# Kernel optimization log

Measured on AMD Instinct MI355X. Metric: run time of the kernel, lower is better.

Reference implementation:

```python
import jax, jax.numpy as jnp
import numpy as np

B, P, M, N, H = 2, 2048, 1024, 16, 64
NEG = 1e10


def setup_inputs() -> dict:
    key = jax.random.key(0)
    ks = jax.random.split(key, 8)
    std = 0.02
    return {
        "x": jax.random.normal(ks[0], (B, P, M), jnp.float32),
        "kernel_query": std * jax.random.normal(ks[1], (N, M, H), jnp.float32),
        "bias_query": jnp.zeros((N, H), jnp.float32),
        "kernel_key": std * jax.random.normal(ks[2], (N, M, H), jnp.float32),
        "bias_key": jnp.zeros((N, H), jnp.float32),
        "kernel_value": std * jax.random.normal(ks[3], (N, M, H), jnp.float32),
        "bias_value": jnp.zeros((N, H), jnp.float32),
        "kernel_out": std * jax.random.normal(ks[4], (N, H, M), jnp.float32),
        "bias_out": jnp.zeros((M,), jnp.float32),
    }


def reference(x, kernel_query, bias_query, kernel_key, bias_key,
              kernel_value, bias_value, kernel_out, bias_out):
    # per-head projections: [b,p,m] x [n,m,h] -> [b,p,n,h]
    q = jnp.einsum('bpm,nmh->bpnh', x, kernel_query) + bias_query
    k = jnp.einsum('bpm,nmh->bpnh', x, kernel_key) + bias_key
    v = jnp.einsum('bpm,nmh->bpnh', x, kernel_value) + bias_value

    # explicit score matrix [b,n,pq,pk]
    scores = jnp.einsum('bqnh,bknh->bnqk', q, k) / jnp.sqrt(jnp.float32(H))
    # faithful reproduction of original (inverted) mask: keep strictly-upper
    # triangle, subtract 1e10 elsewhere
    p = scores.shape[-1]
    mask = jnp.triu(jnp.ones((p, p), scores.dtype), k=1)  # [pq,pk]
    masked = scores * mask - NEG * (1.0 - mask)
    attn = jax.nn.softmax(masked, axis=-1)

    z = jnp.einsum('bknh,bnqk->bqnh', v, attn)
    return jnp.einsum('bqnh,nhm->bqm', z, kernel_out) + bias_out
```

## Files before the change

### kernel.cpp

```cpp
#include <hip/hip_runtime.h>

typedef __attribute__((ext_vector_type(8))) __bf16 bf16x8;
typedef __attribute__((ext_vector_type(4))) float  f32x4;
typedef unsigned short u16;
typedef unsigned int   u32;

__device__ __forceinline__ u16 f2b(float f) {
  u32 u = __builtin_bit_cast(u32, f);
  u32 r = (u + 0x7FFFu + ((u >> 16) & 1u)) >> 16;
  return (u16)r;
}

typedef __attribute__((address_space(3))) void lds_void;
typedef const __attribute__((address_space(1))) void gbl_void;

__device__ __forceinline__ void gload_lds16(const u16* g, u16* l) {
  __builtin_amdgcn_global_load_lds((gbl_void*)g, (lds_void*)l, 16, 0, 0);
}

#define QSCALE 0.18033688011112042f
#define MFIX   4.328085122666891f

__global__ __launch_bounds__(256) void prep_x(const float* __restrict__ x,
                                              u16* __restrict__ xb) {
  int i = blockIdx.x * 256 + threadIdx.x;
  float4 v = ((const float4*)x)[i];
  ushort4 o;
  o.x = f2b(v.x); o.y = f2b(v.y); o.z = f2b(v.z); o.w = f2b(v.w);
  ((ushort4*)xb)[i] = o;
}

__global__ __launch_bounds__(256) void tcast(const float* __restrict__ src,
                                             u16* __restrict__ dst,
                                             int R, int C, int sstride, int dstride,
                                             int smat, int dmat) {
  __shared__ float t[64][65];
  src += (size_t)blockIdx.y * smat;
  dst += (size_t)blockIdx.y * dmat;
  int ntr = R >> 6;
  int rt = blockIdx.x % ntr, ct = blockIdx.x / ntr;
  int r0 = rt * 64, c0 = ct * 64;
  int tid = threadIdx.x;
  int rr = tid >> 2, q = tid & 3;
#pragma unroll
  for (int i = 0; i < 4; ++i) {
    float4 v = *(const float4*)&src[(size_t)(r0 + rr) * sstride + c0 + q * 16 + i * 4];
    t[rr][q * 16 + i * 4 + 0] = v.x;
    t[rr][q * 16 + i * 4 + 1] = v.y;
    t[rr][q * 16 + i * 4 + 2] = v.z;
    t[rr][q * 16 + i * 4 + 3] = v.w;
  }
  __syncthreads();
  int cc = rr;
#pragma unroll
  for (int i = 0; i < 4; ++i) {
    ushort4 o;
    o.x = f2b(t[q * 16 + i * 4 + 0][cc]);
    o.y = f2b(t[q * 16 + i * 4 + 1][cc]);
    o.z = f2b(t[q * 16 + i * 4 + 2][cc]);
    o.w = f2b(t[q * 16 + i * 4 + 3][cc]);
    *(ushort4*)&dst[(size_t)(c0 + cc) * dstride + r0 + q * 16 + i * 4] = o;
  }
}

template <int KDIM>
__device__ __forceinline__ void gemm_main(const u16* __restrict__ A,
                                          const u16* __restrict__ Bm,
                                          int R0, int C0,
                                          u16* As, u16* Bs, f32x4 (&acc)[4][4]) {
  int tid = threadIdx.x;
  int w = tid >> 6, l = tid & 63;
  int lr = l & 15, lg = l >> 4;
  int wr = w >> 1, wc = w & 1;
  for (int k0 = 0; k0 < KDIM; k0 += 32) {
#pragma unroll
    for (int i = 0; i < 2; ++i) {
      int t = w * 2 + i;
      gload_lds16(A  + (size_t)(R0 + t * 16 + (l >> 2)) * KDIM + k0 + (l & 3) * 8, &As[t * 512]);
      gload_lds16(Bm + (size_t)(C0 + t * 16 + (l >> 2)) * KDIM + k0 + (l & 3) * 8, &Bs[t * 512]);
    }
    __syncthreads();
    bf16x8 af[4], bfr[4];
#pragma unroll
    for (int mi = 0; mi < 4; ++mi)
      af[mi] = *(const bf16x8*)&As[(wr * 64 + mi * 16 + lr) * 32 + lg * 8];
#pragma unroll
    for (int ni = 0; ni < 4; ++ni)
      bfr[ni] = *(const bf16x8*)&Bs[(wc * 64 + ni * 16 + lr) * 32 + lg * 8];
#pragma unroll
    for (int mi = 0; mi < 4; ++mi)
#pragma unroll
      for (int ni = 0; ni < 4; ++ni)
        acc[mi][ni] = __builtin_amdgcn_mfma_f32_16x16x32_bf16(af[mi], bfr[ni], acc[mi][ni], 0, 0, 0);
    __syncthreads();
  }
}

__global__ __launch_bounds__(256) void gemm_qkv(const u16* __restrict__ xb,
                                                const u16* __restrict__ wbt,
                                                const float* __restrict__ bq,
                                                const float* __restrict__ bk,
                                                const float* __restrict__ bv,
                                                u16* __restrict__ qb,
                                                u16* __restrict__ kbf,
                                                u16* __restrict__ vtb) {
  __shared__ __align__(16) u16 As[128 * 32];
  __shared__ __align__(16) u16 Bs[128 * 32];
  f32x4 acc[4][4];
#pragma unroll
  for (int mi = 0; mi < 4; ++mi)
#pragma unroll
    for (int ni = 0; ni < 4; ++ni) acc[mi][ni] = (f32x4){0.f, 0.f, 0.f, 0.f};

  int bid = blockIdx.x;
  int rt = bid & 31, ct = bid >> 5;
  int R0 = rt * 128, C0 = ct * 128;
  gemm_main<1024>(xb, wbt, R0, C0, As, Bs, acc);

  int tid = threadIdx.x;
  int w = tid >> 6, l = tid & 63;
  int lr = l & 15, lg = l >> 4;
  int wr = w >> 1, wc = w & 1;
#pragma unroll
  for (int ni = 0; ni < 4; ++ni) {
    int col = C0 + wc * 64 + ni * 16 + lr;
    int proj = col >> 10;
    int within = col & 1023;
    int n = within >> 6, h = within & 63;
    const float* bias = (proj == 0) ? bq : (proj == 1 ? bk : bv);
    float badd = bias[within];
    float scl = (proj == 0) ? QSCALE : 1.0f;
#pragma unroll
    for (int mi = 0; mi < 4; ++mi) {
#pragma unroll
      for (int r = 0; r < 4; ++r) {
        int row = R0 + wr * 64 + mi * 16 + lg * 4 + r;
        int b = row >> 11, p = row & 2047;
        int bn = b * 16 + n;
        u16 u = f2b((acc[mi][ni][r] + badd) * scl);
        if (proj == 0)      qb [((size_t)bn * 2048 + p) * 64 + h] = u;
        else if (proj == 1) kbf[((size_t)bn * 2048 + p) * 64 + h] = u;
        else                vtb[(((size_t)bn * 32 + (p >> 6)) * 64 + h) * 64 + (p & 63)] = u;
      }
    }
  }
}

__global__ __launch_bounds__(256) void mean_v(const u16* __restrict__ vtb,
                                              u16* __restrict__ zb) {
  __shared__ float red[4][64];
  int bn = blockIdx.x;
  int w = threadIdx.x >> 6, h = threadIdx.x & 63;
  const u16* base = vtb + (size_t)bn * 131072 + (size_t)h * 64;
  float acc = 0.f;
  for (int pb = w; pb < 32; pb += 4) {
    const u16* r = base + (size_t)pb * 4096;
#pragma unroll
    for (int c = 0; c < 8; ++c) {
      bf16x8 v = *(const bf16x8*)(r + c * 8);
#pragma unroll
      for (int j = 0; j < 8; ++j) acc += (float)v[j];
    }
  }
  red[w][h] = acc;
  __syncthreads();
  if (w == 0) {
    float s = (red[0][h] + red[1][h] + red[2][h] + red[3][h]) * (1.0f / 2048.0f);
    int b = bn >> 4, n = bn & 15;
    zb[((size_t)(b * 2048 + 2047) * 16 + n) * 64 + h] = f2b(s);
  }
}

#define ATTN_STEP(BUFC, VM, DO_STAGE)                                          \
  {                                                                            \
    asm volatile("s_waitcnt vmcnt(" #VM ")" ::: "memory");                     \
    __builtin_amdgcn_s_barrier();                                              \
    asm volatile("" ::: "memory");                                             \
    f32x4 sacc[4];                                                             \
    __builtin_amdgcn_s_setprio(1);                                             \
    _Pragma("unroll") for (int nb = 0; nb < 4; ++nb) {                         \
      int row = nb * 16 + lr, sw = row & 7;                                    \
      bf16x8 kf0 = *(const bf16x8*)&Ks[BUFC][row * 64 + ((lg ^ sw) << 3)];     \
      bf16x8 kf1 = *(const bf16x8*)&Ks[BUFC][row * 64 + (((lg + 4) ^ sw) << 3)]; \
      f32x4 s = (f32x4){0.f, 0.f, 0.f, 0.f};                                   \
      s = __builtin_amdgcn_mfma_f32_16x16x32_bf16(qf0, kf0, s, 0, 0, 0);       \
      s = __builtin_amdgcn_mfma_f32_16x16x32_bf16(qf1, kf1, s, 0, 0, 0);       \
      sacc[nb] = s;                                                            \
    }                                                                          \
    __builtin_amdgcn_s_setprio(0);                                             \
    u16 pbv[4][4];                                                             \
    if (kb < q0w + 16) {                                                       \
      _Pragma("unroll") for (int nb = 0; nb < 4; ++nb) {                       \
        int key = kb + nb * 16 + lr;                                           \
        _Pragma("unroll") for (int r = 0; r < 4; ++r) {                        \
          int qrow = q0w + lg * 4 + r;                                         \
          float xv = (key > qrow) ? sacc[nb][r] : -1.0e10f;                    \
          float pe = __builtin_amdgcn_exp2f(xv - MFIX);                        \
          rsum[r] += pe;                                                       \
          pbv[nb][r] = __builtin_bit_cast(u16, (__bf16)pe);                    \
        }                                                                      \
      }                                                                        \
    } else {                                                                   \
      _Pragma("unroll") for (int nb = 0; nb < 4; ++nb)                         \
        _Pragma("unroll") for (int r = 0; r < 4; ++r) {                        \
          float pe = __builtin_amdgcn_exp2f(sacc[nb][r] - MFIX);               \
          rsum[r] += pe;                                                       \
          pbv[nb][r] = __builtin_bit_cast(u16, (__bf16)pe);                    \
        }                                                                      \
    }                                                                          \
    _Pragma("unroll") for (int nb = 0; nb < 4; ++nb)                           \
      _Pragma("unroll") for (int r = 0; r < 4; ++r)                            \
        Plds[w][lg * 4 + r][nb * 16 + lr] = pbv[nb][r];                        \
    asm volatile("s_waitcnt lgkmcnt(0)" ::: "memory");                         \
    __builtin_amdgcn_sched_barrier(0);                                         \
    bf16x8 pf0 = *(const bf16x8*)&Plds[w][lr][lg * 8];                         \
    bf16x8 pf1 = *(const bf16x8*)&Plds[w][lr][32 + lg * 8];                    \
    __builtin_amdgcn_s_setprio(1);                                             \
    _Pragma("unroll") for (int hb = 0; hb < 4; ++hb) {                         \
      int row = hb * 16 + lr, sw = row & 7;                                    \
      bf16x8 vf0 = *(const bf16x8*)&Vs[BUFC][row * 64 + ((lg ^ sw) << 3)];     \
      bf16x8 vf1 = *(const bf16x8*)&Vs[BUFC][row * 64 + (((lg + 4) ^ sw) << 3)]; \
      oacc[hb] = __builtin_amdgcn_mfma_f32_16x16x32_bf16(pf0, vf0, oacc[hb], 0, 0, 0); \
      oacc[hb] = __builtin_amdgcn_mfma_f32_16x16x32_bf16(pf1, vf1, oacc[hb], 0, 0, 0); \
    }                                                                          \
    __builtin_amdgcn_s_setprio(0);                                             \
    if (t == tA - 1) {                                                         \
      finalize(q0w);                                                           \
      q0w = cB * 64 + w * 16;                                                  \
      qf0 = *(const bf16x8*)&Q[(size_t)(q0w + lr) * 64 + lg * 8];              \
      qf1 = *(const bf16x8*)&Q[(size_t)(q0w + lr) * 64 + 32 + lg * 8];         \
      _Pragma("unroll") for (int r = 0; r < 4; ++r) rsum[r] = 0.0f;            \
      _Pragma("unroll") for (int hb = 0; hb < 4; ++hb)                         \
        oacc[hb] = (f32x4){0.f, 0.f, 0.f, 0.f};                                \
      kb = cB * 64 - 64;                                                       \
    }                                                                          \
    asm volatile("" ::: "memory");                                             \
    __builtin_amdgcn_s_barrier();                                              \
    if (DO_STAGE) {                                                            \
      if (t + 3 == tA) {                                                       \
        sk = Kp + (size_t)cB * 4096 + soff;                                    \
        sv = Vt + (size_t)cB * 4096 + soff;                                    \
      }                                                                        \
      gload_lds16(sk,       &Ks[BUFC][w * 1024]);                              \
      gload_lds16(sk + 512, &Ks[BUFC][w * 1024 + 512]);                        \
      gload_lds16(sv,       &Vs[BUFC][w * 1024]);                              \
      gload_lds16(sv + 512, &Vs[BUFC][w * 1024 + 512]);                        \
      sk += 4096; sv += 4096;                                                  \
    }                                                                          \
    kb += 64; ++t;                                                             \
  }

__global__ __launch_bounds__(256) void attn_kern(const u16* __restrict__ qb,
                                                 const u16* __restrict__ kbf,
                                                 const u16* __restrict__ vtb,
                                                 u16* __restrict__ zb) {
  __shared__ __align__(16) u16 Ks[3][4096];
  __shared__ __align__(16) u16 Vs[3][4096];
  __shared__ __align__(16) u16 Plds[4][16][72];

  int bid = blockIdx.x;
  int bn = bid & 31, p = bid >> 5;
  int tid = threadIdx.x;
  int w = tid >> 6, l = tid & 63;
  int lr = l & 15, lg = l >> 4;

  int cA = p, cB = 31 - p;
  int tA = 32 - p;

  const u16* Q  = qb  + (size_t)bn * 131072;
  const u16* Kp = kbf + (size_t)bn * 131072;
  const u16* Vt = vtb + (size_t)bn * 131072;

  int row0 = w * 16 + (l >> 3), col8 = l & 7;
  int soff = row0 * 64 + ((col8 ^ (row0 & 7)) << 3);

  int q0w = cA * 64 + w * 16;
  bf16x8 qf0 = *(const bf16x8*)&Q[(size_t)(q0w + lr) * 64 + lg * 8];
  bf16x8 qf1 = *(const bf16x8*)&Q[(size_t)(q0w + lr) * 64 + 32 + lg * 8];

  float rsum[4];
  f32x4 oacc[4];
#pragma unroll
  for (int r = 0; r < 4; ++r) rsum[r] = 0.0f;
#pragma unroll
  for (int hb = 0; hb < 4; ++hb) oacc[hb] = (f32x4){0.f, 0.f, 0.f, 0.f};

  auto finalize = [&](int q0) {
#pragma unroll
    for (int r = 0; r < 4; ++r) {
      float v = rsum[r];
      v += __shfl_xor(v, 1);
      v += __shfl_xor(v, 2);
      v += __shfl_xor(v, 4);
      v += __shfl_xor(v, 8);
      rsum[r] = 1.0f / v;
    }
    int b = bn >> 4, n = bn & 15;
#pragma unroll
    for (int hb = 0; hb < 4; ++hb) {
      int h = hb * 16 + lr;
#pragma unroll
      for (int r = 0; r < 4; ++r) {
        int qrow = q0 + lg * 4 + r;
        zb[((size_t)(b * 2048 + qrow) * 16 + n) * 64 + h] = f2b(oacc[hb][r] * rsum[r]);
      }
    }
  };

  const u16* sk = Kp + (size_t)cA * 4096 + soff;
  const u16* sv = Vt + (size_t)cA * 4096 + soff;
#pragma unroll
  for (int i = 0; i < 3; ++i) {
    gload_lds16(sk,       &Ks[i][w * 1024]);
    gload_lds16(sk + 512, &Ks[i][w * 1024 + 512]);
    gload_lds16(sv,       &Vs[i][w * 1024]);
    gload_lds16(sv + 512, &Vs[i][w * 1024 + 512]);
    sk += 4096; sv += 4096;
  }

  int t = 0;
  int kb = cA * 64;
  for (int it = 0; it < 10; ++it) {
    ATTN_STEP(0, 8, true)
    ATTN_STEP(1, 8, true)
    ATTN_STEP(2, 8, true)
  }
  ATTN_STEP(0, 8, false)
  ATTN_STEP(1, 4, false)
  ATTN_STEP(2, 0, false)
  finalize(q0w);
}

__global__ __launch_bounds__(256) void gemm_out(const u16* __restrict__ zb,
                                                const u16* __restrict__ wot,
                                                const float* __restrict__ bo,
                                                float* __restrict__ out) {
  __shared__ __align__(16) u16 As[128 * 32];
  __shared__ __align__(16) u16 Bs[128 * 32];
  f32x4 acc[4][4];
#pragma unroll
  for (int mi = 0; mi < 4; ++mi)
#pragma unroll
    for (int ni = 0; ni < 4; ++ni) acc[mi][ni] = (f32x4){0.f, 0.f, 0.f, 0.f};

  int bid = blockIdx.x;
  int rt = bid & 31, ct = bid >> 5;
  int R0 = rt * 128, C0 = ct * 128;
  gemm_main<1024>(zb, wot, R0, C0, As, Bs, acc);

  int tid = threadIdx.x;
  int w = tid >> 6, l = tid & 63;
  int lr = l & 15, lg = l >> 4;
  int wr = w >> 1, wc = w & 1;
#pragma unroll
  for (int ni = 0; ni < 4; ++ni) {
    int col = C0 + wc * 64 + ni * 16 + lr;
    float badd = bo[col];
#pragma unroll
    for (int mi = 0; mi < 4; ++mi) {
#pragma unroll
      for (int r = 0; r < 4; ++r) {
        int row = R0 + wr * 64 + mi * 16 + lg * 4 + r;
        out[(size_t)row * 1024 + col] = acc[mi][ni][r] + badd;
      }
    }
  }
}

extern "C" void kernel_launch(void* const* d_in, const int* in_sizes, int n_in,
                              void* d_out, int out_size, void* d_ws, size_t ws_size,
                              hipStream_t stream) {
  const float* x  = (const float*)d_in[0];
  const float* wq = (const float*)d_in[1];
  const float* bq = (const float*)d_in[2];
  const float* wk = (const float*)d_in[3];
  const float* bk = (const float*)d_in[4];
  const float* wv = (const float*)d_in[5];
  const float* bv = (const float*)d_in[6];
  const float* wo = (const float*)d_in[7];
  const float* bo = (const float*)d_in[8];
  float* out = (float*)d_out;

  char* ws = (char*)d_ws;
  u16* xb  = (u16*)(ws + ((size_t)0 << 20));
  u16* wbt = (u16*)(ws + ((size_t)8 << 20));
  u16* wot = (u16*)(ws + ((size_t)14 << 20));
  u16* qb  = (u16*)(ws + ((size_t)16 << 20));
  u16* kbf = (u16*)(ws + ((size_t)24 << 20));
  u16* vtb = (u16*)(ws + ((size_t)32 << 20));
  u16* zb  = (u16*)(ws + ((size_t)40 << 20));

  prep_x<<<dim3(4096), dim3(256), 0, stream>>>(x, xb);
  tcast<<<dim3(16, 16), dim3(256), 0, stream>>>(wq, wbt + (0u << 20), 1024, 64, 64, 1024, 65536, 65536);
  tcast<<<dim3(16, 16), dim3(256), 0, stream>>>(wk, wbt + (1u << 20), 1024, 64, 64, 1024, 65536, 65536);
  tcast<<<dim3(16, 16), dim3(256), 0, stream>>>(wv, wbt + (2u << 20), 1024, 64, 64, 1024, 65536, 65536);
  tcast<<<dim3(256, 1), dim3(256), 0, stream>>>(wo, wot, 1024, 1024, 1024, 1024, 0, 0);

  gemm_qkv<<<dim3(32 * 24), dim3(256), 0, stream>>>(xb, wbt, bq, bk, bv, qb, kbf, vtb);
  attn_kern<<<dim3(512), dim3(256), 0, stream>>>(qb, kbf, vtb, zb);
  mean_v<<<dim3(32), dim3(256), 0, stream>>>(vtb, zb);
  gemm_out<<<dim3(32 * 8), dim3(256), 0, stream>>>(zb, wot, bo, out);
}
```

Baseline: 131.4 us.

## Split paired-chunk attention blocks into one block per query chunk with double buffering

```diff
diff --git a/kernel.cpp b/kernel.cpp
--- a/kernel.cpp
+++ b/kernel.cpp
@@ -171,9 +171,18 @@
   }
 }
 
-#define ATTN_STEP(BUFC, VM, DO_STAGE)                                          \
+#define ATTN_STEP(BUFC, MASKED)                                                \
   {                                                                            \
-    asm volatile("s_waitcnt vmcnt(" #VM ")" ::: "memory");                     \
+    if (t + 1 < trips) {                                                       \
+      gload_lds16(sk,       &Ks[BUFC ^ 1][w * 1024]);                          \
+      gload_lds16(sk + 512, &Ks[BUFC ^ 1][w * 1024 + 512]);                    \
+      gload_lds16(sv,       &Vs[BUFC ^ 1][w * 1024]);                          \
+      gload_lds16(sv + 512, &Vs[BUFC ^ 1][w * 1024 + 512]);                    \
+      sk += 4096; sv += 4096;                                                  \
+      asm volatile("s_waitcnt vmcnt(4)" ::: "memory");                         \
+    } else {                                                                   \
+      asm volatile("s_waitcnt vmcnt(0)" ::: "memory");                         \
+    }                                                                          \
     __builtin_amdgcn_s_barrier();                                              \
     asm volatile("" ::: "memory");                                             \
     f32x4 sacc[4];                                                             \
@@ -189,11 +198,11 @@
     }                                                                          \
     __builtin_amdgcn_s_setprio(0);                                             \
     u16 pbv[4][4];                                                             \
-    if (kb < q0w + 16) {                                                       \
+    if (MASKED) {                                                              \
       _Pragma("unroll") for (int nb = 0; nb < 4; ++nb) {                       \
-        int key = kb + nb * 16 + lr;                                           \
+        int key = nb * 16 + lr;                                                \
         _Pragma("unroll") for (int r = 0; r < 4; ++r) {                        \
-          int qrow = q0w + lg * 4 + r;                                         \
+          int qrow = w * 16 + lg * 4 + r;                                      \
           float xv = (key > qrow) ? sacc[nb][r] : -1.0e10f;                    \
           float pe = __builtin_amdgcn_exp2f(xv - MFIX);                        \
           rsum[r] += pe;                                                       \
@@ -209,12 +218,14 @@
         }                                                                      \
     }                                                                          \
     _Pragma("unroll") for (int nb = 0; nb < 4; ++nb)                           \
-      _Pragma("unroll") for (int r = 0; r < 4; ++r)                            \
-        Plds[w][lg * 4 + r][nb * 16 + lr] = pbv[nb][r];                        \
+      _Pragma("unroll") for (int r = 0; r < 4; ++r) {                          \
+        int prow = lg * 4 + r;                                                 \
+        Plds[w][prow * 64 + ((((nb * 2) + (lr >> 3)) ^ (prow & 7)) << 3) + (lr & 7)] = pbv[nb][r]; \
+      }                                                                        \
     asm volatile("s_waitcnt lgkmcnt(0)" ::: "memory");                         \
     __builtin_amdgcn_sched_barrier(0);                                         \
-    bf16x8 pf0 = *(const bf16x8*)&Plds[w][lr][lg * 8];                         \
-    bf16x8 pf1 = *(const bf16x8*)&Plds[w][lr][32 + lg * 8];                    \
+    bf16x8 pf0 = *(const bf16x8*)&Plds[w][lr * 64 + ((lg ^ (lr & 7)) << 3)];   \
+    bf16x8 pf1 = *(const bf16x8*)&Plds[w][lr * 64 + (((4 + lg) ^ (lr & 7)) << 3)]; \
     __builtin_amdgcn_s_setprio(1);                                             \
     _Pragma("unroll") for (int hb = 0; hb < 4; ++hb) {                         \
       int row = hb * 16 + lr, sw = row & 7;                                    \
@@ -224,48 +235,25 @@
       oacc[hb] = __builtin_amdgcn_mfma_f32_16x16x32_bf16(pf1, vf1, oacc[hb], 0, 0, 0); \
     }                                                                          \
     __builtin_amdgcn_s_setprio(0);                                             \
-    if (t == tA - 1) {                                                         \
-      finalize(q0w);                                                           \
-      q0w = cB * 64 + w * 16;                                                  \
-      qf0 = *(const bf16x8*)&Q[(size_t)(q0w + lr) * 64 + lg * 8];              \
-      qf1 = *(const bf16x8*)&Q[(size_t)(q0w + lr) * 64 + 32 + lg * 8];         \
-      _Pragma("unroll") for (int r = 0; r < 4; ++r) rsum[r] = 0.0f;            \
-      _Pragma("unroll") for (int hb = 0; hb < 4; ++hb)                         \
-        oacc[hb] = (f32x4){0.f, 0.f, 0.f, 0.f};                                \
-      kb = cB * 64 - 64;                                                       \
-    }                                                                          \
     asm volatile("" ::: "memory");                                             \
     __builtin_amdgcn_s_barrier();                                              \
-    if (DO_STAGE) {                                                            \
-      if (t + 3 == tA) {                                                       \
-        sk = Kp + (size_t)cB * 4096 + soff;                                    \
-        sv = Vt + (size_t)cB * 4096 + soff;                                    \
-      }                                                                        \
-      gload_lds16(sk,       &Ks[BUFC][w * 1024]);                              \
-      gload_lds16(sk + 512, &Ks[BUFC][w * 1024 + 512]);                        \
-      gload_lds16(sv,       &Vs[BUFC][w * 1024]);                              \
-      gload_lds16(sv + 512, &Vs[BUFC][w * 1024 + 512]);                        \
-      sk += 4096; sv += 4096;                                                  \
-    }                                                                          \
-    kb += 64; ++t;                                                             \
-  }
-
-__global__ __launch_bounds__(256) void attn_kern(const u16* __restrict__ qb,
-                                                 const u16* __restrict__ kbf,
-                                                 const u16* __restrict__ vtb,
-                                                 u16* __restrict__ zb) {
-  __shared__ __align__(16) u16 Ks[3][4096];
-  __shared__ __align__(16) u16 Vs[3][4096];
-  __shared__ __align__(16) u16 Plds[4][16][72];
+    ++t;                                                                       \
+  }
+
+__global__ __launch_bounds__(256, 4) void attn_kern(const u16* __restrict__ qb,
+                                                    const u16* __restrict__ kbf,
+                                                    const u16* __restrict__ vtb,
+                                                    u16* __restrict__ zb) {
+  __shared__ __align__(16) u16 Ks[2][4096];
+  __shared__ __align__(16) u16 Vs[2][4096];
+  __shared__ __align__(16) u16 Plds[4][1024];
 
   int bid = blockIdx.x;
-  int bn = bid & 31, p = bid >> 5;
+  int bn = bid & 31, c = bid >> 5;
+  int trips = 32 - c;
   int tid = threadIdx.x;
   int w = tid >> 6, l = tid & 63;
   int lr = l & 15, lg = l >> 4;
-
-  int cA = p, cB = 31 - p;
-  int tA = 32 - p;
 
   const u16* Q  = qb  + (size_t)bn * 131072;
   const u16* Kp = kbf + (size_t)bn * 131072;
@@ -274,7 +262,7 @@
   int row0 = w * 16 + (l >> 3), col8 = l & 7;
   int soff = row0 * 64 + ((col8 ^ (row0 & 7)) << 3);
 
-  int q0w = cA * 64 + w * 16;
+  int q0w = c * 64 + w * 16;
   bf16x8 qf0 = *(const bf16x8*)&Q[(size_t)(q0w + lr) * 64 + lg * 8];
   bf16x8 qf1 = *(const bf16x8*)&Q[(size_t)(q0w + lr) * 64 + 32 + lg * 8];
 
@@ -285,50 +273,41 @@
 #pragma unroll
   for (int hb = 0; hb < 4; ++hb) oacc[hb] = (f32x4){0.f, 0.f, 0.f, 0.f};
 
-  auto finalize = [&](int q0) {
+  const u16* sk = Kp + (size_t)c * 4096 + soff;
+  const u16* sv = Vt + (size_t)c * 4096 + soff;
+  gload_lds16(sk,       &Ks[0][w * 1024]);
+  gload_lds16(sk + 512, &Ks[0][w * 1024 + 512]);
+  gload_lds16(sv,       &Vs[0][w * 1024]);
+  gload_lds16(sv + 512, &Vs[0][w * 1024 + 512]);
+  sk += 4096; sv += 4096;
+
+  int t = 0;
+  ATTN_STEP(0, true)
+  while (t + 1 < trips) {
+    ATTN_STEP(1, false)
+    ATTN_STEP(0, false)
+  }
+  if (t < trips) ATTN_STEP(1, false)
+
+#pragma unroll
+  for (int r = 0; r < 4; ++r) {
+    float v = rsum[r];
+    v += __shfl_xor(v, 1);
+    v += __shfl_xor(v, 2);
+    v += __shfl_xor(v, 4);
+    v += __shfl_xor(v, 8);
+    rsum[r] = 1.0f / v;
+  }
+  int b = bn >> 4, n = bn & 15;
+#pragma unroll
+  for (int hb = 0; hb < 4; ++hb) {
+    int h = hb * 16 + lr;
 #pragma unroll
     for (int r = 0; r < 4; ++r) {
-      float v = rsum[r];
-      v += __shfl_xor(v, 1);
-      v += __shfl_xor(v, 2);
-      v += __shfl_xor(v, 4);
-      v += __shfl_xor(v, 8);
-      rsum[r] = 1.0f / v;
-    }
-    int b = bn >> 4, n = bn & 15;
-#pragma unroll
-    for (int hb = 0; hb < 4; ++hb) {
-      int h = hb * 16 + lr;
-#pragma unroll
-      for (int r = 0; r < 4; ++r) {
-        int qrow = q0 + lg * 4 + r;
-        zb[((size_t)(b * 2048 + qrow) * 16 + n) * 64 + h] = f2b(oacc[hb][r] * rsum[r]);
-      }
-    }
-  };
-
-  const u16* sk = Kp + (size_t)cA * 4096 + soff;
-  const u16* sv = Vt + (size_t)cA * 4096 + soff;
-#pragma unroll
-  for (int i = 0; i < 3; ++i) {
-    gload_lds16(sk,       &Ks[i][w * 1024]);
-    gload_lds16(sk + 512, &Ks[i][w * 1024 + 512]);
-    gload_lds16(sv,       &Vs[i][w * 1024]);
-    gload_lds16(sv + 512, &Vs[i][w * 1024 + 512]);
-    sk += 4096; sv += 4096;
-  }
-
-  int t = 0;
-  int kb = cA * 64;
-  for (int it = 0; it < 10; ++it) {
-    ATTN_STEP(0, 8, true)
-    ATTN_STEP(1, 8, true)
-    ATTN_STEP(2, 8, true)
-  }
-  ATTN_STEP(0, 8, false)
-  ATTN_STEP(1, 4, false)
-  ATTN_STEP(2, 0, false)
-  finalize(q0w);
+      int qrow = q0w + lg * 4 + r;
+      zb[((size_t)(b * 2048 + qrow) * 16 + n) * 64 + h] = f2b(oacc[hb][r] * rsum[r]);
+    }
+  }
 }
 
 __global__ __launch_bounds__(256) void gemm_out(const u16* __restrict__ zb,
@@ -397,7 +376,7 @@
   tcast<<<dim3(256, 1), dim3(256), 0, stream>>>(wo, wot, 1024, 1024, 1024, 1024, 0, 0);
 
   gemm_qkv<<<dim3(32 * 24), dim3(256), 0, stream>>>(xb, wbt, bq, bk, bv, qb, kbf, vtb);
-  attn_kern<<<dim3(512), dim3(256), 0, stream>>>(qb, kbf, vtb, zb);
+  attn_kern<<<dim3(1024), dim3(256), 0, stream>>>(qb, kbf, vtb, zb);
   mean_v<<<dim3(32), dim3(256), 0, stream>>>(vtb, zb);
   gemm_out<<<dim3(32 * 8), dim3(256), 0, stream>>>(zb, wot, bo, out);
 }
```

Result: faster. 128.0 us (-2.6%).
